# Kernel tuning notes

Hardware: AMD Instinct MI355X
Metric: run time of the kernel (lower is better)

The kernel has to match this reference:

```python
import jax, jax.numpy as jnp
import numpy as np

N = 50000      # nodes
E = 400000     # edges
D = 256        # args.dimensions
H1 = 32        # hidden1 (per-head)
HEADS = 4      # gat_heads
H2 = 64        # hidden2
DEC = 512      # decoder1
B = 4096       # number of entity index pairs
NEG = 0.2      # PyG GATConv leaky_relu negative slope


def setup_inputs() -> dict:
    key = jax.random.key(0)
    ks = jax.random.split(key, 24)
    s = lambda k, shape, fan: jax.random.normal(k, shape, jnp.float32) * (1.0 / np.sqrt(fan))
    return {
        "x_o": jax.random.normal(ks[0], (N, D), jnp.float32),
        "x_a": jax.random.normal(ks[1], (N, D), jnp.float32),
        "edge_index": jax.random.randint(ks[2], (2, E), 0, N, jnp.int32),
        "idx": jax.random.randint(ks[3], (2, B), 0, N, jnp.int32),
        # GATConv 1: in D -> H1 per head, HEADS heads, concat
        "W1": s(ks[4], (D, HEADS * H1), D),
        "a_src1": s(ks[5], (HEADS, H1), H1),
        "a_dst1": s(ks[6], (HEADS, H1), H1),
        "b1": jnp.zeros((HEADS * H1,), jnp.float32),
        "p1": jnp.full((HEADS * H1,), 0.25, jnp.float32),   # PReLU weight
        # GATConv 2: HEADS*H1 -> H2, 1 head, no concat
        "W2": s(ks[7], (HEADS * H1, H2), HEADS * H1),
        "a_src2": s(ks[8], (1, H2), H2),
        "a_dst2": s(ks[9], (1, H2), H2),
        "b2": jnp.zeros((H2,), jnp.float32),
        "p2": jnp.full((H2,), 0.25, jnp.float32),
        # mlp1
        "mlp_W": s(ks[10], (H2, H2), H2),
        "mlp_b": jnp.zeros((H2,), jnp.float32),
        # Discriminator bilinear (out=1)
        "disc_W": s(ks[11], (H2, H2), H2),
        "disc_b": jnp.zeros((), jnp.float32),
        # adversarial_logits linear (fixed, deterministic stand-in)
        "adv_W": s(ks[12], (H2, H2), H2),
        "adv_b": jnp.zeros((H2,), jnp.float32),
        # fusion decoder (stand-in for build_fusion_decoder): MLP with 2 heads
        "f_W1": s(ks[13], (2 * H2, DEC), 2 * H2),
        "f_b1": jnp.zeros((DEC,), jnp.float32),
        "f_W2": s(ks[14], (DEC, 2), DEC),
        "f_b2": jnp.zeros((2,), jnp.float32),
        "f_W3": s(ks[15], (DEC, 2), DEC),
        "f_b3": jnp.zeros((2,), jnp.float32),
    }


def prelu(x, w):
    return jnp.where(x >= 0, x, w * x)


def gat_conv(x, src, dst, W, a_src, a_dst, b, heads, out_dim, concat):
    # PyG GATConv (eval): per-head linear, edge attention, dst-segment softmax, scatter-sum.
    n = x.shape[0]
    h = (x @ W).reshape(n, heads, out_dim)                  # [N, H, F]
    a_s = (h * a_src[None]).sum(-1)                         # [N, H]
    a_d = (h * a_dst[None]).sum(-1)                         # [N, H]
    e = jax.nn.leaky_relu(a_s[src] + a_d[dst], NEG)         # [E', H]
    e_max = jax.ops.segment_max(e, dst, num_segments=n)
    w = jnp.exp(e - e_max[dst])
    denom = jax.ops.segment_sum(w, dst, num_segments=n)
    alpha = w / (denom[dst] + 1e-16)                        # [E', H]
    out = jax.ops.segment_sum(h[src] * alpha[..., None], dst, num_segments=n)  # [N, H, F]
    out = out.reshape(n, heads * out_dim) if concat else out.mean(1)
    return out + b


def encode(x, src, dst, W1, a_src1, a_dst1, b1, p1, W2, a_src2, a_dst2, b2, p2):
    x1 = prelu(gat_conv(x, src, dst, W1, a_src1, a_dst1, b1, HEADS, H1, True), p1)
    x2 = gat_conv(x1, src, dst, W2, a_src2, a_dst2, b2, 1, H2, False)
    return prelu(x2, p2)


def discriminate(c, h_pl, h_mi, disc_W, disc_b):
    # nn.Bilinear(n_h, n_h, 1) against broadcast summary c
    Wc = disc_W @ c                                          # [H2]
    sc_1 = h_pl @ Wc + disc_b                                # [N]
    sc_2 = h_mi @ Wc + disc_b                                # [N]
    return jnp.stack([sc_1, sc_2], axis=1)                   # [N, 2]


def reference(x_o, x_a, edge_index, idx,
              W1, a_src1, a_dst1, b1, p1,
              W2, a_src2, a_dst2, b2, p2,
              mlp_W, mlp_b, disc_W, disc_b, adv_W, adv_b,
              f_W1, f_b1, f_W2, f_b2, f_W3, f_b3):
    n = x_o.shape[0]
    loops = jnp.arange(n, dtype=edge_index.dtype)            # PyG add_self_loops=True
    src = jnp.concatenate([edge_index[0], loops])
    dst = jnp.concatenate([edge_index[1], loops])

    x2_o = encode(x_o, src, dst, W1, a_src1, a_dst1, b1, p1, W2, a_src2, a_dst2, b2, p2)
    x2_o_a = encode(x_a, src, dst, W1, a_src1, a_dst1, b1, p1, W2, a_src2, a_dst2, b2, p2)

    h_os = jax.nn.sigmoid(x2_o.mean(0)) @ mlp_W + mlp_b      # AvgReadout -> sigmoid -> mlp1
    h_os_a = jax.nn.sigmoid(x2_o_a.mean(0)) @ mlp_W + mlp_b

    ret_os = discriminate(h_os, x2_o, x2_o_a, disc_W, disc_b)
    ret_os_a = discriminate(h_os_a, x2_o_a, x2_o, disc_W, disc_b)

    # entities (task_type 'other' branch)
    e1 = x2_o[idx[0]]
    e2 = x2_o[idx[1]]
    fh = jax.nn.relu(jnp.concatenate([e1, e2], axis=-1) @ f_W1 + f_b1)
    log = fh @ f_W2 + f_b2
    log1 = fh @ f_W3 + f_b3

    sc_1 = (x2_o @ adv_W + adv_b).sum(1)[None, :]            # [1, N]
    sc_2 = (x2_o_a @ adv_W + adv_b).sum(1)[None, :]
    logits = jnp.concatenate([sc_1, sc_2], axis=1)           # [1, 2N]

    return (log, ret_os, ret_os_a, x2_o, logits, log1)
```

## Files before the change

### kernel.cpp

```cpp
#include <hip/hip_runtime.h>
#include <hip/hip_bf16.h>
#include <math.h>

constexpr int NN   = 50000;
constexpr int N2   = 2*NN;
constexpr int EE   = 400000;
constexpr int DIN  = 256;
constexpr int M1   = 128;
constexpr int H1N  = 4;
constexpr int M2   = 64;
constexpr int BP   = 4096;
constexpr int DEC  = 512;
constexpr float SLOPE = 0.2f;

constexpr int O_LOG    = 0;
constexpr int O_RETOS  = 8192;
constexpr int O_RETOSA = 108192;
constexpr int O_X2     = 208192;
constexpr int O_LOGITS = 3408192;
constexpr int O_LOG1   = 3508192;

constexpr int SCAN_NB = (NN + 1023) / 1024;

typedef __attribute__((ext_vector_type(8))) short short8;
typedef __attribute__((ext_vector_type(4))) float f32x4;

__device__ __forceinline__ short f2bs(float v){
    __hip_bfloat16 h = __float2bfloat16(v);
    unsigned short u; __builtin_memcpy(&u, &h, 2);
    return (short)u;
}
__device__ __forceinline__ float lrelu(float e){ return (e >= 0.f) ? e : SLOPE*e; }

__global__ void hist_dst(const int* __restrict__ edst, int* __restrict__ cnt){
    int i = blockIdx.x*blockDim.x + threadIdx.x;
    if (i < EE) atomicAdd(&cnt[edst[i]], 1);
}

__global__ __launch_bounds__(1024) void scan_blk(const int* __restrict__ cnt,
                                                 int* __restrict__ rowex,
                                                 int* __restrict__ bsum){
    __shared__ int wsum[16];
    const int t = threadIdx.x;
    const int idx = blockIdx.x*1024 + t;
    const int lane = t & 63, wid = t >> 6;
    int v = (idx < NN) ? cnt[idx] : 0;
    int s = v;
    #pragma unroll
    for (int o = 1; o < 64; o <<= 1){
        int u = __shfl_up(s, o, 64);
        if (lane >= o) s += u;
    }
    if (lane == 63) wsum[wid] = s;
    __syncthreads();
    if (wid == 0){
        int ws = (lane < 16) ? wsum[lane] : 0;
        #pragma unroll
        for (int o = 1; o < 16; o <<= 1){
            int u = __shfl_up(ws, o, 64);
            if (lane >= o) ws += u;
        }
        if (lane < 16) wsum[lane] = ws;
    }
    __syncthreads();
    int base = (wid > 0) ? wsum[wid-1] : 0;
    int incl = base + s;
    if (idx < NN) rowex[idx] = incl - v;
    if (t == 1023) bsum[blockIdx.x] = incl;
}

__global__ void scan_bsum(int* __restrict__ bsum, int nb){
    const int lane = threadIdx.x;
    int v = (lane < nb) ? bsum[lane] : 0;
    int s = v;
    #pragma unroll
    for (int o = 1; o < 64; o <<= 1){
        int u = __shfl_up(s, o, 64);
        if (lane >= o) s += u;
    }
    if (lane < nb) bsum[lane] = s - v;
}

__global__ void scan_fix(int* __restrict__ row, const int* __restrict__ bsum,
                         int* __restrict__ cursor){
    int idx = blockIdx.x*blockDim.x + threadIdx.x;
    if (idx < NN){
        int r = row[idx] + bsum[idx >> 10];
        row[idx] = r;
        cursor[idx] = r;
    }
    if (idx == 0) row[NN] = EE;
}

__global__ void fill_csr(const int* __restrict__ esrc, const int* __restrict__ edst,
                         int* __restrict__ cursor, int* __restrict__ adj){
    int i = blockIdx.x*blockDim.x + threadIdx.x;
    if (i >= EE) return;
    int d = edst[i];
    int slot = atomicAdd(&cursor[d], 1);
    adj[slot] = esrc[i];
}

__device__ __forceinline__ void pack_one(const float* __restrict__ W,
                                         __hip_bfloat16* __restrict__ Wpk,
                                         int i, int M){
    int k = i / M, c = i - k*M;
    int kb = k >> 5, r = k & 31, quad = r >> 3, j = r & 7;
    int ct = c >> 4, ln = quad*16 + (c & 15);
    int CT = M >> 4;
    size_t dst = (((size_t)kb*CT + ct)*64 + ln)*8 + j;
    Wpk[dst] = __float2bfloat16(W[i]);
}

__global__ void pack_all(const float* __restrict__ W1, const float* __restrict__ W2,
                         const float* __restrict__ fW1,
                         __hip_bfloat16* __restrict__ Wpk1,
                         __hip_bfloat16* __restrict__ Wpk2,
                         __hip_bfloat16* __restrict__ Wpkf){
    constexpr int S1 = DIN*M1;
    constexpr int S2 = S1 + M1*M2;
    constexpr int S3 = S2 + M1*DEC;
    int i = blockIdx.x*blockDim.x + threadIdx.x;
    if (i < S1)       pack_one(W1,  Wpk1, i,      M1);
    else if (i < S2)  pack_one(W2,  Wpk2, i - S1, M2);
    else if (i < S3)  pack_one(fW1, Wpkf, i - S2, DEC);
}

template<int K, int M, int HEADS_T, bool AF32>
__global__ __launch_bounds__(256) void gemm_attn(
        const void* __restrict__ X0, const void* __restrict__ X1,
        const __hip_bfloat16* __restrict__ Wpk,
        const float* __restrict__ asrc, const float* __restrict__ adst,
        __hip_bfloat16* __restrict__ Hb,
        float* __restrict__ AS, float* __restrict__ AD){
    constexpr int CT = M/16;
    constexpr int KB = K/32;
    constexpr int CPH = CT/HEADS_T;
    const int wave = (blockIdx.x*256 + threadIdx.x) >> 6;
    const int lane = threadIdx.x & 63;
    const int n0 = wave*16;
    if (n0 >= N2) return;
    const int arow = lane & 15;
    const int quad = lane >> 4;

    f32x4 acc[CT];
    #pragma unroll
    for (int ct = 0; ct < CT; ++ct) acc[ct] = (f32x4){0.f,0.f,0.f,0.f};

    const float* apf = nullptr;
    const __hip_bfloat16* apb = nullptr;
    if constexpr (AF32){
        apf = (n0 < NN) ? ((const float*)X0 + (size_t)(n0 + arow)*K)
                        : ((const float*)X1 + (size_t)(n0 - NN + arow)*K);
    } else {
        apb = (const __hip_bfloat16*)X0 + (size_t)(n0 + arow)*K;
    }

    for (int kb = 0; kb < KB; ++kb){
        const int kbase = kb*32 + quad*8;
        short8 af;
        if constexpr (AF32){
            float4 v0 = *(const float4*)(apf + kbase);
            float4 v1 = *(const float4*)(apf + kbase + 4);
            af[0]=f2bs(v0.x); af[1]=f2bs(v0.y); af[2]=f2bs(v0.z); af[3]=f2bs(v0.w);
            af[4]=f2bs(v1.x); af[5]=f2bs(v1.y); af[6]=f2bs(v1.z); af[7]=f2bs(v1.w);
        } else {
            af = *(const short8*)(apb + kbase);
        }
        const __hip_bfloat16* wp = Wpk + (size_t)kb*CT*64*8;
        #pragma unroll
        for (int ct = 0; ct < CT; ++ct){
            short8 bfr = *(const short8*)(wp + ((size_t)ct*64 + lane)*8);
            acc[ct] = __builtin_amdgcn_mfma_f32_16x16x32_bf16(af, bfr, acc[ct], 0, 0, 0);
        }
    }

    #pragma unroll
    for (int ct = 0; ct < CT; ++ct){
        #pragma unroll
        for (int r = 0; r < 4; ++r){
            int n = n0 + quad*4 + r;
            Hb[(size_t)n*M + ct*16 + arow] = __float2bfloat16(acc[ct][r]);
        }
    }

    float a_s[CT], a_d[CT];
    #pragma unroll
    for (int ct = 0; ct < CT; ++ct){
        a_s[ct] = asrc[ct*16 + arow];
        a_d[ct] = adst[ct*16 + arow];
    }
    #pragma unroll
    for (int r = 0; r < 4; ++r){
        const int n = n0 + quad*4 + r;
        #pragma unroll
        for (int h = 0; h < HEADS_T; ++h){
            float ss = 0.f, dd = 0.f;
            #pragma unroll
            for (int c2 = 0; c2 < CPH; ++c2){
                int ct = h*CPH + c2;
                ss += acc[ct][r]*a_s[ct];
                dd += acc[ct][r]*a_d[ct];
            }
            #pragma unroll
            for (int o = 8; o > 0; o >>= 1){
                ss += __shfl_down(ss, o, 16);
                dd += __shfl_down(dd, o, 16);
            }
            if (arow == 0){
                AS[(size_t)n*HEADS_T + h] = ss;
                AD[(size_t)n*HEADS_T + h] = dd;
            }
        }
    }
}

__global__ __launch_bounds__(256) void gat_agg_l1(
        const int* __restrict__ row, const int* __restrict__ adj,
        const __hip_bfloat16* __restrict__ Hfeat,
        const float* __restrict__ AS, const float* __restrict__ AD,
        const float* __restrict__ b, const float* __restrict__ p,
        __hip_bfloat16* __restrict__ outB){
    const int wv = (blockIdx.x*blockDim.x + threadIdx.x) >> 6;
    const int nw = (gridDim.x*blockDim.x) >> 6;
    const int t = threadIdx.x & 63;
    const int h = t >> 4;
    const unsigned* Hw = (const unsigned*)Hfeat;
    const float bb0 = b[2*t], bb1 = b[2*t+1];
    const float pp0 = p[2*t], pp1 = p[2*t+1];
    for (int nd = wv; nd < N2; nd += nw){
        const int g  = (nd < NN) ? nd : nd - NN;
        const int fb = nd - g;
        const float ad_h = AD[(size_t)nd*4 + h];
        float acc0, acc1, den;
        {
            float ws = __expf(lrelu(AS[(size_t)nd*4 + h] + ad_h));
            unsigned u = Hw[(size_t)nd*64 + t];
            acc0 = __uint_as_float(u << 16) * ws;
            acc1 = __uint_as_float(u & 0xffff0000u) * ws;
            den = ws;
        }
        const int beg = row[g], end = row[g+1];
        int j = beg;
        for (; j + 7 < end; j += 8){
            int s0 = adj[j]   + fb; int s1 = adj[j+1] + fb;
            int s2 = adj[j+2] + fb; int s3 = adj[j+3] + fb;
            int s4 = adj[j+4] + fb; int s5 = adj[j+5] + fb;
            int s6 = adj[j+6] + fb; int s7 = adj[j+7] + fb;
            float e0 = AS[(size_t)s0*4 + h]; float e1 = AS[(size_t)s1*4 + h];
            float e2 = AS[(size_t)s2*4 + h]; float e3 = AS[(size_t)s3*4 + h];
            float e4 = AS[(size_t)s4*4 + h]; float e5 = AS[(size_t)s5*4 + h];
            float e6 = AS[(size_t)s6*4 + h]; float e7 = AS[(size_t)s7*4 + h];
            unsigned u0 = Hw[(size_t)s0*64 + t]; unsigned u1 = Hw[(size_t)s1*64 + t];
            unsigned u2 = Hw[(size_t)s2*64 + t]; unsigned u3 = Hw[(size_t)s3*64 + t];
            unsigned u4 = Hw[(size_t)s4*64 + t]; unsigned u5 = Hw[(size_t)s5*64 + t];
            unsigned u6 = Hw[(size_t)s6*64 + t]; unsigned u7 = Hw[(size_t)s7*64 + t];
            float w0 = __expf(lrelu(e0 + ad_h)); float w1 = __expf(lrelu(e1 + ad_h));
            float w2 = __expf(lrelu(e2 + ad_h)); float w3 = __expf(lrelu(e3 + ad_h));
            float w4 = __expf(lrelu(e4 + ad_h)); float w5 = __expf(lrelu(e5 + ad_h));
            float w6 = __expf(lrelu(e6 + ad_h)); float w7 = __expf(lrelu(e7 + ad_h));
            acc0 += __uint_as_float(u0 << 16) * w0;
            acc1 += __uint_as_float(u0 & 0xffff0000u) * w0;
            acc0 += __uint_as_float(u1 << 16) * w1;
            acc1 += __uint_as_float(u1 & 0xffff0000u) * w1;
            acc0 += __uint_as_float(u2 << 16) * w2;
            acc1 += __uint_as_float(u2 & 0xffff0000u) * w2;
            acc0 += __uint_as_float(u3 << 16) * w3;
            acc1 += __uint_as_float(u3 & 0xffff0000u) * w3;
            acc0 += __uint_as_float(u4 << 16) * w4;
            acc1 += __uint_as_float(u4 & 0xffff0000u) * w4;
            acc0 += __uint_as_float(u5 << 16) * w5;
            acc1 += __uint_as_float(u5 & 0xffff0000u) * w5;
            acc0 += __uint_as_float(u6 << 16) * w6;
            acc1 += __uint_as_float(u6 & 0xffff0000u) * w6;
            acc0 += __uint_as_float(u7 << 16) * w7;
            acc1 += __uint_as_float(u7 & 0xffff0000u) * w7;
            den += w0 + w1 + w2 + w3 + w4 + w5 + w6 + w7;
        }
        for (; j + 3 < end; j += 4){
            int s0 = adj[j]   + fb; int s1 = adj[j+1] + fb;
            int s2 = adj[j+2] + fb; int s3 = adj[j+3] + fb;
            float e0 = AS[(size_t)s0*4 + h]; float e1 = AS[(size_t)s1*4 + h];
            float e2 = AS[(size_t)s2*4 + h]; float e3 = AS[(size_t)s3*4 + h];
            unsigned u0 = Hw[(size_t)s0*64 + t]; unsigned u1 = Hw[(size_t)s1*64 + t];
            unsigned u2 = Hw[(size_t)s2*64 + t]; unsigned u3 = Hw[(size_t)s3*64 + t];
            float w0 = __expf(lrelu(e0 + ad_h)); float w1 = __expf(lrelu(e1 + ad_h));
            float w2 = __expf(lrelu(e2 + ad_h)); float w3 = __expf(lrelu(e3 + ad_h));
            acc0 += __uint_as_float(u0 << 16) * w0;
            acc1 += __uint_as_float(u0 & 0xffff0000u) * w0;
            acc0 += __uint_as_float(u1 << 16) * w1;
            acc1 += __uint_as_float(u1 & 0xffff0000u) * w1;
            acc0 += __uint_as_float(u2 << 16) * w2;
            acc1 += __uint_as_float(u2 & 0xffff0000u) * w2;
            acc0 += __uint_as_float(u3 << 16) * w3;
            acc1 += __uint_as_float(u3 & 0xffff0000u) * w3;
            den += w0 + w1 + w2 + w3;
        }
        for (; j < end; ++j){
            int s = adj[j] + fb;
            float wgt = __expf(lrelu(AS[(size_t)s*4 + h] + ad_h));
            unsigned u = Hw[(size_t)s*64 + t];
            acc0 += __uint_as_float(u << 16) * wgt;
            acc1 += __uint_as_float(u & 0xffff0000u) * wgt;
            den += wgt;
        }
        float inv = 1.f/(den + 1e-16f);
        float v0 = acc0*inv + bb0;
        float v1 = acc1*inv + bb1;
        v0 = (v0 >= 0.f) ? v0 : pp0*v0;
        v1 = (v1 >= 0.f) ? v1 : pp1*v1;
        ushort2 st = make_ushort2((unsigned short)f2bs(v0), (unsigned short)f2bs(v1));
        *(ushort2*)(outB + (size_t)nd*128 + 2*t) = st;
    }
}

__global__ __launch_bounds__(256) void gat_agg_l2(
        const int* __restrict__ row, const int* __restrict__ adj,
        const __hip_bfloat16* __restrict__ Hfeat,
        const float* __restrict__ AS, const float* __restrict__ AD,
        const float* __restrict__ b, const float* __restrict__ p,
        float* __restrict__ outO, float* __restrict__ outA){
    const int wv = (blockIdx.x*blockDim.x + threadIdx.x) >> 6;
    const int nw = (gridDim.x*blockDim.x) >> 6;
    const int t = threadIdx.x & 63;
    const float bb = b[t], pp = p[t];
    const ushort* Hu = (const ushort*)Hfeat;
    for (int nd = wv; nd < N2; nd += nw){
        const int g  = (nd < NN) ? nd : nd - NN;
        const int fb = nd - g;
        const float ad_d = AD[nd];
        float acc, den;
        {
            float ws = __expf(lrelu(AS[nd] + ad_d));
            unsigned u = Hu[(size_t)nd*64 + t];
            acc = __uint_as_float(u << 16) * ws;
            den = ws;
        }
        const int beg = row[g], end = row[g+1];
        int j = beg;
        for (; j + 7 < end; j += 8){
            int s0 = adj[j]   + fb; int s1 = adj[j+1] + fb;
            int s2 = adj[j+2] + fb; int s3 = adj[j+3] + fb;
            int s4 = adj[j+4] + fb; int s5 = adj[j+5] + fb;
            int s6 = adj[j+6] + fb; int s7 = adj[j+7] + fb;
            float e0 = AS[s0]; float e1 = AS[s1];
            float e2 = AS[s2]; float e3 = AS[s3];
            float e4 = AS[s4]; float e5 = AS[s5];
            float e6 = AS[s6]; float e7 = AS[s7];
            unsigned u0 = Hu[(size_t)s0*64 + t]; unsigned u1 = Hu[(size_t)s1*64 + t];
            unsigned u2 = Hu[(size_t)s2*64 + t]; unsigned u3 = Hu[(size_t)s3*64 + t];
            unsigned u4 = Hu[(size_t)s4*64 + t]; unsigned u5 = Hu[(size_t)s5*64 + t];
            unsigned u6 = Hu[(size_t)s6*64 + t]; unsigned u7 = Hu[(size_t)s7*64 + t];
            float w0 = __expf(lrelu(e0 + ad_d)); float w1 = __expf(lrelu(e1 + ad_d));
            float w2 = __expf(lrelu(e2 + ad_d)); float w3 = __expf(lrelu(e3 + ad_d));
            float w4 = __expf(lrelu(e4 + ad_d)); float w5 = __expf(lrelu(e5 + ad_d));
            float w6 = __expf(lrelu(e6 + ad_d)); float w7 = __expf(lrelu(e7 + ad_d));
            acc += __uint_as_float(u0 << 16) * w0;
            acc += __uint_as_float(u1 << 16) * w1;
            acc += __uint_as_float(u2 << 16) * w2;
            acc += __uint_as_float(u3 << 16) * w3;
            acc += __uint_as_float(u4 << 16) * w4;
            acc += __uint_as_float(u5 << 16) * w5;
            acc += __uint_as_float(u6 << 16) * w6;
            acc += __uint_as_float(u7 << 16) * w7;
            den += w0 + w1 + w2 + w3 + w4 + w5 + w6 + w7;
        }
        for (; j + 3 < end; j += 4){
            int s0 = adj[j]   + fb; int s1 = adj[j+1] + fb;
            int s2 = adj[j+2] + fb; int s3 = adj[j+3] + fb;
            float e0 = AS[s0]; float e1 = AS[s1];
            float e2 = AS[s2]; float e3 = AS[s3];
            unsigned u0 = Hu[(size_t)s0*64 + t]; unsigned u1 = Hu[(size_t)s1*64 + t];
            unsigned u2 = Hu[(size_t)s2*64 + t]; unsigned u3 = Hu[(size_t)s3*64 + t];
            float w0 = __expf(lrelu(e0 + ad_d)); float w1 = __expf(lrelu(e1 + ad_d));
            float w2 = __expf(lrelu(e2 + ad_d)); float w3 = __expf(lrelu(e3 + ad_d));
            acc += __uint_as_float(u0 << 16) * w0;
            acc += __uint_as_float(u1 << 16) * w1;
            acc += __uint_as_float(u2 << 16) * w2;
            acc += __uint_as_float(u3 << 16) * w3;
            den += w0 + w1 + w2 + w3;
        }
        for (; j < end; ++j){
            int s = adj[j] + fb;
            float wgt = __expf(lrelu(AS[s] + ad_d));
            unsigned u = Hu[(size_t)s*64 + t];
            acc += __uint_as_float(u << 16) * wgt;
            den += wgt;
        }
        float v = acc/(den + 1e-16f) + bb;
        v = (v >= 0.f) ? v : pp*v;
        if (nd < NN) outO[(size_t)nd*64 + t] = v;
        else         outA[(size_t)(nd - NN)*64 + t] = v;
    }
}

__global__ __launch_bounds__(256) void colsum2(const float* __restrict__ Xo,
                                               const float* __restrict__ Xa,
                                               float* __restrict__ outO,
                                               float* __restrict__ outA){
    __shared__ float red[2][256];
    const int t = threadIdx.x;
    const int c = t & 63;
    const int rg = t >> 6;
    float so = 0.f, sa = 0.f;
    for (int r = blockIdx.x*4 + rg; r < NN; r += gridDim.x*4){
        so += Xo[(size_t)r*64 + c];
        sa += Xa[(size_t)r*64 + c];
    }
    red[0][t] = so; red[1][t] = sa; __syncthreads();
    if (t < 64){
        atomicAdd(&outO[c], red[0][t] + red[0][t+64] + red[0][t+128] + red[0][t+192]);
        atomicAdd(&outA[c], red[1][t] + red[1][t+64] + red[1][t+128] + red[1][t+192]);
    }
}

__global__ void summary(const float* __restrict__ csum_o, const float* __restrict__ csum_a,
                        const float* __restrict__ mlpW, const float* __restrict__ mlpb,
                        const float* __restrict__ discW,
                        const float* __restrict__ advW, const float* __restrict__ advb,
                        float* __restrict__ Wc_o, float* __restrict__ Wc_a,
                        float* __restrict__ advRow, float* __restrict__ advbsum){
    __shared__ float s_o[64], s_a[64], h_o[64], h_a[64];
    const int t = threadIdx.x;
    s_o[t] = 1.f/(1.f + expf(-csum_o[t]/(float)NN));
    s_a[t] = 1.f/(1.f + expf(-csum_a[t]/(float)NN));
    __syncthreads();
    float ao = 0.f, aa = 0.f;
    for (int k = 0; k < 64; ++k){ float w = mlpW[k*64 + t]; ao += s_o[k]*w; aa += s_a[k]*w; }
    float bb = mlpb[t];
    h_o[t] = ao + bb; h_a[t] = aa + bb;
    __syncthreads();
    float wo = 0.f, wa = 0.f;
    for (int j = 0; j < 64; ++j){ float w = discW[t*64 + j]; wo += w*h_o[j]; wa += w*h_a[j]; }
    Wc_o[t] = wo; Wc_a[t] = wa;
    float ar = 0.f;
    for (int j = 0; j < 64; ++j) ar += advW[t*64 + j];
    advRow[t] = ar;
    float ab = advb[t];
    for (int o = 32; o > 0; o >>= 1) ab += __shfl_down(ab, o, 64);
    if (t == 0) advbsum[0] = ab;
}

__global__ void node_outputs(const float* __restrict__ x2o, const float* __restrict__ x2a,
                             const float* __restrict__ Wc_o, const float* __restrict__ Wc_a,
                             const float* __restrict__ advRow, const float* __restrict__ advbsum,
                             const float* __restrict__ discb,
                             float* __restrict__ out){
    const int n = blockIdx.x*4 + (threadIdx.x >> 6);
    const int l = threadIdx.x & 63;
    float xo = x2o[(size_t)n*64 + l], xa = x2a[(size_t)n*64 + l];
    float wo = Wc_o[l], wa = Wc_a[l], ar = advRow[l];
    float d1 = xo*wo, d2 = xa*wo, d3 = xa*wa, d4 = xo*wa, d5 = xo*ar, d6 = xa*ar;
    for (int o = 32; o > 0; o >>= 1){
        d1 += __shfl_down(d1, o, 64); d2 += __shfl_down(d2, o, 64);
        d3 += __shfl_down(d3, o, 64); d4 += __shfl_down(d4, o, 64);
        d5 += __shfl_down(d5, o, 64); d6 += __shfl_down(d6, o, 64);
    }
    if (l == 0){
        float db = discb[0];
        float ab = advbsum[0];
        out[O_RETOS  + n*2 + 0] = d1 + db;
        out[O_RETOS  + n*2 + 1] = d2 + db;
        out[O_RETOSA + n*2 + 0] = d3 + db;
        out[O_RETOSA + n*2 + 1] = d4 + db;
        out[O_LOGITS + n]       = d5 + ab;
        out[O_LOGITS + NN + n]  = d6 + ab;
    }
}

__global__ __launch_bounds__(256) void decoder_fused(
        const float* __restrict__ x2o, const int* __restrict__ idxArr,
        const __hip_bfloat16* __restrict__ Wpkf, const float* __restrict__ fb1,
        const float* __restrict__ fW2, const float* __restrict__ fb2,
        const float* __restrict__ fW3, const float* __restrict__ fb3,
        float* __restrict__ out){
    __shared__ float part[4][16][4];
    const int t = threadIdx.x;
    const int wid = t >> 6, lane = t & 63;
    const int arow = lane & 15, quad = lane >> 4;
    const int p0 = blockIdx.x*16;
    const int i0 = idxArr[p0 + arow];
    const int i1 = idxArr[BP + p0 + arow];

    f32x4 acc[8];
    #pragma unroll
    for (int c = 0; c < 8; ++c) acc[c] = (f32x4){0.f,0.f,0.f,0.f};

    #pragma unroll
    for (int kb = 0; kb < 4; ++kb){
        int src = (kb < 2) ? i0 : i1;
        int koff = (kb & 1)*32 + quad*8;
        const float* ap = x2o + (size_t)src*64 + koff;
        float4 v0 = *(const float4*)ap;
        float4 v1 = *(const float4*)(ap + 4);
        short8 af;
        af[0]=f2bs(v0.x); af[1]=f2bs(v0.y); af[2]=f2bs(v0.z); af[3]=f2bs(v0.w);
        af[4]=f2bs(v1.x); af[5]=f2bs(v1.y); af[6]=f2bs(v1.z); af[7]=f2bs(v1.w);
        const __hip_bfloat16* wp = Wpkf + (size_t)kb*32*64*8;
        #pragma unroll
        for (int c = 0; c < 8; ++c){
            int ct = wid*8 + c;
            short8 bfr = *(const short8*)(wp + ((size_t)ct*64 + lane)*8);
            acc[c] = __builtin_amdgcn_mfma_f32_16x16x32_bf16(af, bfr, acc[c], 0, 0, 0);
        }
    }

    float a0[4] = {0,0,0,0}, a1[4] = {0,0,0,0};
    float c0[4] = {0,0,0,0}, c1[4] = {0,0,0,0};
    #pragma unroll
    for (int c = 0; c < 8; ++c){
        int col = wid*128 + c*16 + arow;
        float bb = fb1[col];
        float w20 = fW2[col*2], w21 = fW2[col*2+1];
        float w30 = fW3[col*2], w31 = fW3[col*2+1];
        #pragma unroll
        for (int r = 0; r < 4; ++r){
            float v = acc[c][r] + bb;
            v = (v > 0.f) ? v : 0.f;
            a0[r] += v*w20; a1[r] += v*w21;
            c0[r] += v*w30; c1[r] += v*w31;
        }
    }
    #pragma unroll
    for (int o = 8; o > 0; o >>= 1){
        #pragma unroll
        for (int r = 0; r < 4; ++r){
            a0[r] += __shfl_down(a0[r], o, 16);
            a1[r] += __shfl_down(a1[r], o, 16);
            c0[r] += __shfl_down(c0[r], o, 16);
            c1[r] += __shfl_down(c1[r], o, 16);
        }
    }
    if (arow == 0){
        #pragma unroll
        for (int r = 0; r < 4; ++r){
            part[wid][quad*4 + r][0] = a0[r];
            part[wid][quad*4 + r][1] = a1[r];
            part[wid][quad*4 + r][2] = c0[r];
            part[wid][quad*4 + r][3] = c1[r];
        }
    }
    __syncthreads();
    if (t < 64){
        int pr = t >> 2, o = t & 3;
        float s = part[0][pr][o] + part[1][pr][o] + part[2][pr][o] + part[3][pr][o];
        int gb = p0 + pr;
        if (o == 0)      out[O_LOG  + gb*2 + 0] = s + fb2[0];
        else if (o == 1) out[O_LOG  + gb*2 + 1] = s + fb2[1];
        else if (o == 2) out[O_LOG1 + gb*2 + 0] = s + fb3[0];
        else             out[O_LOG1 + gb*2 + 1] = s + fb3[1];
    }
}

extern "C" void kernel_launch(void* const* d_in, const int* in_sizes, int n_in,
                              void* d_out, int out_size, void* d_ws, size_t ws_size,
                              hipStream_t stream){
    const float* x_o    = (const float*)d_in[0];
    const float* x_a    = (const float*)d_in[1];
    const int*   edge   = (const int*)d_in[2];
    const int*   idxp   = (const int*)d_in[3];
    const float* W1     = (const float*)d_in[4];
    const float* a_src1 = (const float*)d_in[5];
    const float* a_dst1 = (const float*)d_in[6];
    const float* b1     = (const float*)d_in[7];
    const float* p1     = (const float*)d_in[8];
    const float* W2     = (const float*)d_in[9];
    const float* a_src2 = (const float*)d_in[10];
    const float* a_dst2 = (const float*)d_in[11];
    const float* b2     = (const float*)d_in[12];
    const float* p2     = (const float*)d_in[13];
    const float* mlpW   = (const float*)d_in[14];
    const float* mlpb   = (const float*)d_in[15];
    const float* discW  = (const float*)d_in[16];
    const float* discb  = (const float*)d_in[17];
    const float* advW   = (const float*)d_in[18];
    const float* advb   = (const float*)d_in[19];
    const float* fW1    = (const float*)d_in[20];
    const float* fb1    = (const float*)d_in[21];
    const float* fW2    = (const float*)d_in[22];
    const float* fb2    = (const float*)d_in[23];
    const float* fW3    = (const float*)d_in[24];
    const float* fb3    = (const float*)d_in[25];

    const int* esrc = edge;
    const int* edst = edge + EE;

    float* w = (float*)d_ws;
    size_t off = 0;
    auto alloc = [&](size_t nfloats){ float* p = w + off; off += nfloats; return p; };
    __hip_bfloat16* Hb   = (__hip_bfloat16*)alloc((size_t)N2*M1/2);
    __hip_bfloat16* x1b  = (__hip_bfloat16*)alloc((size_t)N2*M1/2);
    float* asb   = alloc((size_t)N2*H1N);
    float* adb   = alloc((size_t)N2*H1N);
    __hip_bfloat16* Wpk1 = (__hip_bfloat16*)alloc((size_t)DIN*M1/2);
    __hip_bfloat16* Wpk2 = (__hip_bfloat16*)alloc((size_t)M1*M2/2);
    __hip_bfloat16* Wpkf = (__hip_bfloat16*)alloc((size_t)M1*DEC/2);
    int*   cnt   = (int*)alloc(NN);
    int*   row   = (int*)alloc(NN + 1);
    int*   cursor= (int*)alloc(NN);
    int*   adj   = (int*)alloc(EE);
    int*   bsum  = (int*)alloc(SCAN_NB + 1);
    float* smallb= alloc(512);
    float* csum_o = smallb;       float* csum_a = smallb + 64;
    float* Wc_o   = smallb + 128; float* Wc_a   = smallb + 192;
    float* advRow = smallb + 256; float* advbs  = smallb + 320;

    float* x2a = (float*)x1b;

    float* out = (float*)d_out;
    float* x2o = out + O_X2;

    hipMemsetAsync(cnt, 0, NN*sizeof(int), stream);
    hipMemsetAsync(smallb, 0, 128*sizeof(float), stream);
    hist_dst<<<(EE + 255)/256, 256, 0, stream>>>(edst, cnt);
    scan_blk<<<SCAN_NB, 1024, 0, stream>>>(cnt, row, bsum);
    scan_bsum<<<1, 64, 0, stream>>>(bsum, SCAN_NB);
    scan_fix<<<(NN + 255)/256, 256, 0, stream>>>(row, bsum, cursor);
    fill_csr<<<(EE + 255)/256, 256, 0, stream>>>(esrc, edst, cursor, adj);
    pack_all<<<(DIN*M1 + M1*M2 + M1*DEC + 255)/256, 256, 0, stream>>>(
        W1, W2, fW1, Wpk1, Wpk2, Wpkf);

    const int gw = ((N2/16) + 3) / 4;

    gemm_attn<DIN, M1, H1N, true><<<gw, 256, 0, stream>>>(
        x_o, x_a, Wpk1, a_src1, a_dst1, Hb, asb, adb);
    gat_agg_l1<<<2048, 256, 0, stream>>>(row, adj, Hb, asb, adb, b1, p1, x1b);

    gemm_attn<M1, M2, 1, false><<<gw, 256, 0, stream>>>(
        x1b, nullptr, Wpk2, a_src2, a_dst2, Hb, asb, adb);
    gat_agg_l2<<<2048, 256, 0, stream>>>(row, adj, Hb, asb, adb, b2, p2, x2o, x2a);

    colsum2<<<256, 256, 0, stream>>>(x2o, x2a, csum_o, csum_a);
    summary<<<1, 64, 0, stream>>>(csum_o, csum_a, mlpW, mlpb, discW, advW, advb,
                                  Wc_o, Wc_a, advRow, advbs);
    node_outputs<<<NN/4, 256, 0, stream>>>(x2o, x2a, Wc_o, Wc_a, advRow, advbs, discb, out);
    decoder_fused<<<BP/16, 256, 0, stream>>>(x2o, idxp, Wpkf, fb1, fW2, fb2, fW3, fb3, out);
}
```

Before: 412.0 us.

## Stage GEMM weights in LDS with persistent waves and A-operand prefetch

The attention GEMM kernel now copies the whole packed weight matrix into shared memory once per block. It then runs a grid-stride loop over 16-row tiles with a fixed, smaller grid, so the weight load is amortised across many tiles. The next K-slice of the activation row is prefetched into registers while MFMAs run on the current slice. This aims to cut repeated global and L2 weight reads and hide activation load latency. In exchange, LDS use is 64 KB per block for layer 1, which caps occupancy to about two blocks per CU, and the kb loop is no longer unrolled.

```diff
diff --git a/kernel.cpp b/kernel.cpp
--- a/kernel.cpp
+++ b/kernel.cpp
@@ -127,7 +127,7 @@
 }
 
 template<int K, int M, int HEADS_T, bool AF32>
-__global__ __launch_bounds__(256) void gemm_attn(
+__global__ __launch_bounds__(256, 2) void gemm_attn(
         const void* __restrict__ X0, const void* __restrict__ X1,
         const __hip_bfloat16* __restrict__ Wpk,
         const float* __restrict__ asrc, const float* __restrict__ adst,
@@ -136,80 +136,109 @@
     constexpr int CT = M/16;
     constexpr int KB = K/32;
     constexpr int CPH = CT/HEADS_T;
-    const int wave = (blockIdx.x*256 + threadIdx.x) >> 6;
-    const int lane = threadIdx.x & 63;
-    const int n0 = wave*16;
-    if (n0 >= N2) return;
-    const int arow = lane & 15;
-    const int quad = lane >> 4;
-
-    f32x4 acc[CT];
-    #pragma unroll
-    for (int ct = 0; ct < CT; ++ct) acc[ct] = (f32x4){0.f,0.f,0.f,0.f};
-
-    const float* apf = nullptr;
-    const __hip_bfloat16* apb = nullptr;
-    if constexpr (AF32){
-        apf = (n0 < NN) ? ((const float*)X0 + (size_t)(n0 + arow)*K)
-                        : ((const float*)X1 + (size_t)(n0 - NN + arow)*K);
-    } else {
-        apb = (const __hip_bfloat16*)X0 + (size_t)(n0 + arow)*K;
-    }
-
-    for (int kb = 0; kb < KB; ++kb){
-        const int kbase = kb*32 + quad*8;
-        short8 af;
+    __shared__ __hip_bfloat16 Wl[K*M];
+
+    {
+        short8* dstv = (short8*)Wl;
+        const short8* srcv = (const short8*)Wpk;
+        for (int i = threadIdx.x; i < K*M/8; i += 256)
+            dstv[i] = srcv[i];
+    }
+    __syncthreads();
+
+    const int wave0 = (blockIdx.x*256 + threadIdx.x) >> 6;
+    const int nwv   = (gridDim.x*256) >> 6;
+    const int lane  = threadIdx.x & 63;
+    const int arow  = lane & 15;
+    const int quad  = lane >> 4;
+
+    for (int tile = wave0; tile*16 < N2; tile += nwv){
+        const int n0 = tile*16;
+
+        const float* apf = nullptr;
+        const __hip_bfloat16* apb = nullptr;
         if constexpr (AF32){
-            float4 v0 = *(const float4*)(apf + kbase);
-            float4 v1 = *(const float4*)(apf + kbase + 4);
-            af[0]=f2bs(v0.x); af[1]=f2bs(v0.y); af[2]=f2bs(v0.z); af[3]=f2bs(v0.w);
-            af[4]=f2bs(v1.x); af[5]=f2bs(v1.y); af[6]=f2bs(v1.z); af[7]=f2bs(v1.w);
+            apf = ((n0 < NN) ? ((const float*)X0 + (size_t)(n0 + arow)*K)
+                             : ((const float*)X1 + (size_t)(n0 - NN + arow)*K)) + quad*8;
         } else {
-            af = *(const short8*)(apb + kbase);
-        }
-        const __hip_bfloat16* wp = Wpk + (size_t)kb*CT*64*8;
+            apb = (const __hip_bfloat16*)X0 + (size_t)(n0 + arow)*K + quad*8;
+        }
+
+        float4 ra0, ra1;
+        short8 rb;
+        if constexpr (AF32){
+            ra0 = *(const float4*)(apf);
+            ra1 = *(const float4*)(apf + 4);
+        } else {
+            rb = *(const short8*)(apb);
+        }
+
+        f32x4 acc[CT];
+        #pragma unroll
+        for (int ct = 0; ct < CT; ++ct) acc[ct] = (f32x4){0.f,0.f,0.f,0.f};
+
+        #pragma unroll 1
+        for (int kb = 0; kb < KB; ++kb){
+            short8 af;
+            if constexpr (AF32){
+                af[0]=f2bs(ra0.x); af[1]=f2bs(ra0.y); af[2]=f2bs(ra0.z); af[3]=f2bs(ra0.w);
+                af[4]=f2bs(ra1.x); af[5]=f2bs(ra1.y); af[6]=f2bs(ra1.z); af[7]=f2bs(ra1.w);
+            } else {
+                af = rb;
+            }
+            if (kb + 1 < KB){
+                const int kn = (kb + 1)*32;
+                if constexpr (AF32){
+                    ra0 = *(const float4*)(apf + kn);
+                    ra1 = *(const float4*)(apf + kn + 4);
+                } else {
+                    rb = *(const short8*)(apb + kn);
+                }
+            }
+            const __hip_bfloat16* wl = Wl + (size_t)kb*CT*64*8;
+            #pragma unroll
+            for (int ct = 0; ct < CT; ++ct){
+                short8 bfr = *(const short8*)(wl + ((size_t)ct*64 + lane)*8);
+                acc[ct] = __builtin_amdgcn_mfma_f32_16x16x32_bf16(af, bfr, acc[ct], 0, 0, 0);
+            }
+        }
+
         #pragma unroll
         for (int ct = 0; ct < CT; ++ct){
-            short8 bfr = *(const short8*)(wp + ((size_t)ct*64 + lane)*8);
-            acc[ct] = __builtin_amdgcn_mfma_f32_16x16x32_bf16(af, bfr, acc[ct], 0, 0, 0);
-        }
-    }
-
-    #pragma unroll
-    for (int ct = 0; ct < CT; ++ct){
+            #pragma unroll
+            for (int r = 0; r < 4; ++r){
+                int n = n0 + quad*4 + r;
+                Hb[(size_t)n*M + ct*16 + arow] = __float2bfloat16(acc[ct][r]);
+            }
+        }
+
+        float a_s[CT], a_d[CT];
+        #pragma unroll
+        for (int ct = 0; ct < CT; ++ct){
+            a_s[ct] = asrc[ct*16 + arow];
+            a_d[ct] = adst[ct*16 + arow];
+        }
         #pragma unroll
         for (int r = 0; r < 4; ++r){
-            int n = n0 + quad*4 + r;
-            Hb[(size_t)n*M + ct*16 + arow] = __float2bfloat16(acc[ct][r]);
-        }
-    }
-
-    float a_s[CT], a_d[CT];
-    #pragma unroll
-    for (int ct = 0; ct < CT; ++ct){
-        a_s[ct] = asrc[ct*16 + arow];
-        a_d[ct] = adst[ct*16 + arow];
-    }
-    #pragma unroll
-    for (int r = 0; r < 4; ++r){
-        const int n = n0 + quad*4 + r;
-        #pragma unroll
-        for (int h = 0; h < HEADS_T; ++h){
-            float ss = 0.f, dd = 0.f;
+            const int n = n0 + quad*4 + r;
             #pragma unroll
-            for (int c2 = 0; c2 < CPH; ++c2){
-                int ct = h*CPH + c2;
-                ss += acc[ct][r]*a_s[ct];
-                dd += acc[ct][r]*a_d[ct];
-            }
-            #pragma unroll
-            for (int o = 8; o > 0; o >>= 1){
-                ss += __shfl_down(ss, o, 16);
-                dd += __shfl_down(dd, o, 16);
-            }
-            if (arow == 0){
-                AS[(size_t)n*HEADS_T + h] = ss;
-                AD[(size_t)n*HEADS_T + h] = dd;
+            for (int h = 0; h < HEADS_T; ++h){
+                float ss = 0.f, dd = 0.f;
+                #pragma unroll
+                for (int c2 = 0; c2 < CPH; ++c2){
+                    int ct = h*CPH + c2;
+                    ss += acc[ct][r]*a_s[ct];
+                    dd += acc[ct][r]*a_d[ct];
+                }
+                #pragma unroll
+                for (int o = 8; o > 0; o >>= 1){
+                    ss += __shfl_down(ss, o, 16);
+                    dd += __shfl_down(dd, o, 16);
+                }
+                if (arow == 0){
+                    AS[(size_t)n*HEADS_T + h] = ss;
+                    AD[(size_t)n*HEADS_T + h] = dd;
+                }
             }
         }
     }
@@ -620,13 +649,11 @@
     pack_all<<<(DIN*M1 + M1*M2 + M1*DEC + 255)/256, 256, 0, stream>>>(
         W1, W2, fW1, Wpk1, Wpk2, Wpkf);
 
-    const int gw = ((N2/16) + 3) / 4;
-
-    gemm_attn<DIN, M1, H1N, true><<<gw, 256, 0, stream>>>(
+    gemm_attn<DIN, M1, H1N, true><<<512, 256, 0, stream>>>(
         x_o, x_a, Wpk1, a_src1, a_dst1, Hb, asb, adb);
     gat_agg_l1<<<2048, 256, 0, stream>>>(row, adj, Hb, asb, adb, b1, p1, x1b);
 
-    gemm_attn<M1, M2, 1, false><<<gw, 256, 0, stream>>>(
+    gemm_attn<M1, M2, 1, false><<<1024, 256, 0, stream>>>(
         x1b, nullptr, Wpk2, a_src2, a_dst2, Hb, asb, adb);
     gat_agg_l2<<<2048, 256, 0, stream>>>(row, adj, Hb, asb, adb, b2, p2, x2o, x2a);
 
```

After: 408.7 us. Within noise of the previous version (-0.8%).
